# Optimization experiments

Hardware: AMD Instinct MI355X
Metric: run time of the kernel (lower is better)

Reference implementation:

```python
import jax, jax.numpy as jnp
import numpy as np

N_NODES = 50000
N_EDGES = 1600000
IN_C, HID_C, OUT_C = 64, 64, 7


def setup_inputs() -> dict:
    key = jax.random.key(0)
    ks = jax.random.split(key, 8)
    x = jax.random.normal(ks[0], (N_NODES, IN_C), dtype=jnp.float32)
    edge_index = jax.random.randint(ks[1], (2, N_EDGES), 0, N_NODES, dtype=jnp.int64)
    s_in = 1.0 / np.sqrt(IN_C)
    s_hid = 1.0 / np.sqrt(HID_C)
    W1 = jax.random.normal(ks[2], (HID_C, IN_C), dtype=jnp.float32) * s_in
    b1 = jnp.zeros((HID_C,), dtype=jnp.float32)
    W2 = jax.random.normal(ks[3], (HID_C, HID_C), dtype=jnp.float32) * s_hid
    b2 = jnp.zeros((HID_C,), dtype=jnp.float32)
    W3 = jax.random.normal(ks[4], (OUT_C, HID_C), dtype=jnp.float32) * s_hid
    b3 = jnp.zeros((OUT_C,), dtype=jnp.float32)
    return {"x": x, "edge_index": edge_index, "W1": W1, "b1": b1,
            "W2": W2, "b2": b2, "W3": W3, "b3": b3}


def _gcn_conv(x, src, dst, W, b):
    # GCNConv(normalize=False): lin -> sum-aggregate over incoming edges -> +bias
    h = x @ W.T                                   # [N, out]
    msg = h[src]                                  # gather source features [E, out]
    agg = jax.ops.segment_sum(msg, dst, num_segments=N_NODES)  # scatter-add
    return agg + b


def reference(x, edge_index, W1, b1, W2, b2, W3, b3):
    src, dst = edge_index[0], edge_index[1]
    h = jax.nn.relu(_gcn_conv(x, src, dst, W1, b1))   # dropout is identity in eval
    h = jax.nn.relu(_gcn_conv(h, src, dst, W2, b2))
    h = _gcn_conv(h, src, dst, W3, b3)
    return jax.nn.log_softmax(h, axis=-1)
```

## Files before the change

### kernel.cpp

```cpp
#include <hip/hip_runtime.h>
#include <math.h>

#define N_NODES 50000
#define N_EDGES 1600000
#define C 64
#define OUTC 7

#define NB 196
#define BCAP 10240
#define CHUNK 4096

__device__ __forceinline__ unsigned int pk_bf16(float a, float b) {
    unsigned int ua = __float_as_uint(a);
    ua = (ua + 0x7FFFu + ((ua >> 16) & 1u)) >> 16;
    unsigned int ub = __float_as_uint(b);
    ub = (ub + 0x7FFFu + ((ub >> 16) & 1u)) >> 16;
    return ua | (ub << 16);
}

__global__ __launch_bounds__(256) void bin_kernel(const int* __restrict__ src,
                                                  const int* __restrict__ dst,
                                                  unsigned int* __restrict__ buckets,
                                                  int* __restrict__ gcursor) {
    __shared__ unsigned int staged[CHUNK];
    __shared__ int hist[NB], scanb[NB], cur[NB], baseb[NB];
    const int tid = threadIdx.x;
    const int base = blockIdx.x * CHUNK;
    int n = N_EDGES - base; if (n > CHUNK) n = CHUNK;

    for (int b = tid; b < NB; b += 256) { hist[b] = 0; cur[b] = 0; }
    __syncthreads();

    const int4* src4 = (const int4*)(src + base);
    const int4* dst4 = (const int4*)(dst + base);
    unsigned int v[16];
    int nv = n >> 2;
#pragma unroll
    for (int k = 0; k < 4; ++k) {
        int i4 = k * 256 + tid;
        if (i4 < nv) {
            int4 s4 = src4[i4];
            int4 d4 = dst4[i4];
            unsigned int d0 = (unsigned int)d4.x, d1 = (unsigned int)d4.y;
            unsigned int d2 = (unsigned int)d4.z, d3 = (unsigned int)d4.w;
            v[k * 4 + 0] = (d0 << 16) | (unsigned int)s4.x;
            v[k * 4 + 1] = (d1 << 16) | (unsigned int)s4.y;
            v[k * 4 + 2] = (d2 << 16) | (unsigned int)s4.z;
            v[k * 4 + 3] = (d3 << 16) | (unsigned int)s4.w;
            atomicAdd(&hist[d0 >> 8], 1);
            atomicAdd(&hist[d1 >> 8], 1);
            atomicAdd(&hist[d2 >> 8], 1);
            atomicAdd(&hist[d3 >> 8], 1);
        }
    }
    __syncthreads();
    if (tid == 0) {
        int run = 0;
        for (int b = 0; b < NB; ++b) { scanb[b] = run; run += hist[b]; }
    }
    __syncthreads();
#pragma unroll
    for (int k = 0; k < 4; ++k) {
        int i4 = k * 256 + tid;
        if (i4 < nv) {
#pragma unroll
            for (int q = 0; q < 4; ++q) {
                unsigned int w = v[k * 4 + q];
                int b = w >> 24;
                int p = scanb[b] + atomicAdd(&cur[b], 1);
                staged[p] = w;
            }
        }
    }
    __syncthreads();
    if (tid < NB) baseb[tid] = atomicAdd(&gcursor[tid], hist[tid]);
    __syncthreads();
    for (int i = tid; i < n; i += 256) {
        unsigned int w = staged[i];
        int b = w >> 24;
        buckets[(size_t)b * BCAP + baseb[b] + (i - scanb[b])] = w;
    }
}

__global__ __launch_bounds__(256) void build_csr(const unsigned int* __restrict__ buckets,
                                                 const int* __restrict__ gcursor,
                                                 unsigned int* __restrict__ csr,
                                                 int* __restrict__ off) {
    __shared__ int hist[256], part[256], offx[256], cur[256];
    __shared__ int gl[NB];
    __shared__ int s_cnt, s_base;
    const int tid = threadIdx.x;
    const int b = blockIdx.x;

    hist[tid] = 0;
    cur[tid] = 0;
    if (tid < NB) gl[tid] = gcursor[tid];
    __syncthreads();
    if (tid == 0) {
        int bs = 0;
        for (int i = 0; i < b; ++i) bs += gl[i];
        s_base = bs;
        s_cnt = gl[b];
    }
    __syncthreads();
    const int cnt = s_cnt;
    const int gbase = s_base;
    const unsigned int* bk = buckets + (size_t)b * BCAP;

    for (int i = tid; i < cnt; i += 256) {
        atomicAdd(&hist[(bk[i] >> 16) & 255], 1);
    }
    __syncthreads();
    part[tid] = hist[tid];
    __syncthreads();
    for (int d = 1; d < 256; d <<= 1) {
        int t = (tid >= d) ? part[tid - d] : 0;
        __syncthreads();
        part[tid] += t;
        __syncthreads();
    }
    offx[tid] = (tid == 0) ? 0 : part[tid - 1];
    __syncthreads();
    int node = b * 256 + tid;
    if (node < N_NODES) off[node] = gbase + offx[tid];
    if (b == NB - 1 && tid == 0) off[N_NODES] = gbase + cnt;
    for (int i = tid; i < cnt; i += 256) {
        unsigned int w = bk[i];
        int dl = (w >> 16) & 255;
        int p = offx[dl] + atomicAdd(&cur[dl], 1);
        csr[gbase + p] = w & 0xFFFFu;
    }
}


__global__ __launch_bounds__(256) void linear64_bf16(const float* __restrict__ x,
                                                     const float* __restrict__ W,
                                                     unsigned int* __restrict__ tb) {
    const int cg = blockIdx.x & 3;
    const int r = (blockIdx.x >> 2) * 256 + threadIdx.x;
    if (r >= N_NODES) return;
    float4 xr[16];
    const float4* xp = (const float4*)(x + (size_t)r * 64);
#pragma unroll
    for (int j = 0; j < 16; ++j) xr[j] = xp[j];
    const float* xf = (const float*)xr;

    const float* Wp = W + cg * 16 * 64;
    unsigned int* orow = tb + (size_t)r * 32 + cg * 8;
    for (int c0 = 0; c0 < 16; c0 += 8) {
        float acc[8] = {0.f, 0.f, 0.f, 0.f, 0.f, 0.f, 0.f, 0.f};
#pragma unroll
        for (int k = 0; k < 64; ++k) {
            float xv = xf[k];
#pragma unroll
            for (int j = 0; j < 8; ++j)
                acc[j] += xv * Wp[(c0 + j) * 64 + k];
        }
        uint4 w;
        w.x = pk_bf16(acc[0], acc[1]);
        w.y = pk_bf16(acc[2], acc[3]);
        w.z = pk_bf16(acc[4], acc[5]);
        w.w = pk_bf16(acc[6], acc[7]);
        ((uint4*)orow)[c0 >> 3] = w;
    }
}

__global__ __launch_bounds__(128) void linear7_rows(const float* __restrict__ x,
                                                    const float* __restrict__ W,
                                                    float* __restrict__ out) {
    int r = blockIdx.x * 128 + threadIdx.x;
    if (r >= N_NODES) return;
    float4 xr[16];
    const float4* xp = (const float4*)(x + (size_t)r * 64);
#pragma unroll
    for (int j = 0; j < 16; ++j) xr[j] = xp[j];
    const float* xf = (const float*)xr;

    float acc[7] = {0.f, 0.f, 0.f, 0.f, 0.f, 0.f, 0.f};
#pragma unroll
    for (int k = 0; k < 64; ++k) {
        float xv = xf[k];
#pragma unroll
        for (int j = 0; j < 7; ++j)
            acc[j] += xv * W[j * 64 + k];
    }
    float4* op = (float4*)(out + (size_t)r * 8);
    op[0] = make_float4(acc[0], acc[1], acc[2], acc[3]);
    op[1] = make_float4(acc[4], acc[5], acc[6], 0.f);
}


__global__ __launch_bounds__(256) void gather64b(const int* __restrict__ off,
                                                 const unsigned int* __restrict__ csr_src,
                                                 const unsigned int* __restrict__ tb,
                                                 const float* __restrict__ b,
                                                 float* __restrict__ out,
                                                 int do_relu) {
    int node = blockIdx.x * 4 + (threadIdx.x >> 6);
    if (node >= N_NODES) return;
    const int lane = threadIdx.x & 63;
    const int slot = lane >> 3;
    const int ch8  = lane & 7;
    int e0 = off[node], e1 = off[node + 1];
    const uint4* t4 = (const uint4*)tb;
    float s[8] = {0.f, 0.f, 0.f, 0.f, 0.f, 0.f, 0.f, 0.f};
    for (int e = e0; e < e1; e += 16) {
        int i0 = e + slot;
        int i1 = e + 8 + slot;
        bool p0 = i0 < e1, p1 = i1 < e1;
        unsigned int a0 = csr_src[p0 ? i0 : e];
        unsigned int a1 = csr_src[p1 ? i1 : e];
        uint4 v0 = t4[(size_t)a0 * 8 + ch8];
        uint4 v1 = t4[(size_t)a1 * 8 + ch8];
        if (p0) {
            s[0] += __uint_as_float(v0.x << 16);
            s[1] += __uint_as_float(v0.x & 0xFFFF0000u);
            s[2] += __uint_as_float(v0.y << 16);
            s[3] += __uint_as_float(v0.y & 0xFFFF0000u);
            s[4] += __uint_as_float(v0.z << 16);
            s[5] += __uint_as_float(v0.z & 0xFFFF0000u);
            s[6] += __uint_as_float(v0.w << 16);
            s[7] += __uint_as_float(v0.w & 0xFFFF0000u);
        }
        if (p1) {
            s[0] += __uint_as_float(v1.x << 16);
            s[1] += __uint_as_float(v1.x & 0xFFFF0000u);
            s[2] += __uint_as_float(v1.y << 16);
            s[3] += __uint_as_float(v1.y & 0xFFFF0000u);
            s[4] += __uint_as_float(v1.z << 16);
            s[5] += __uint_as_float(v1.z & 0xFFFF0000u);
            s[6] += __uint_as_float(v1.w << 16);
            s[7] += __uint_as_float(v1.w & 0xFFFF0000u);
        }
    }
#pragma unroll
    for (int d = 8; d <= 32; d <<= 1) {
#pragma unroll
        for (int j = 0; j < 8; ++j) s[j] += __shfl_xor(s[j], d, 64);
    }
    if (lane < 8) {
        const float4 b0 = ((const float4*)b)[ch8 * 2];
        const float4 b1 = ((const float4*)b)[ch8 * 2 + 1];
        float4 r0, r1;
        r0.x = s[0] + b0.x; r0.y = s[1] + b0.y; r0.z = s[2] + b0.z; r0.w = s[3] + b0.w;
        r1.x = s[4] + b1.x; r1.y = s[5] + b1.y; r1.z = s[6] + b1.z; r1.w = s[7] + b1.w;
        if (do_relu) {
            r0.x = fmaxf(r0.x, 0.f); r0.y = fmaxf(r0.y, 0.f);
            r0.z = fmaxf(r0.z, 0.f); r0.w = fmaxf(r0.w, 0.f);
            r1.x = fmaxf(r1.x, 0.f); r1.y = fmaxf(r1.y, 0.f);
            r1.z = fmaxf(r1.z, 0.f); r1.w = fmaxf(r1.w, 0.f);
        }
        float4* orow = (float4*)(out + (size_t)node * 64 + ch8 * 8);
        orow[0] = r0;
        orow[1] = r1;
    }
}

__global__ __launch_bounds__(256) void gather7_lsm(const int* __restrict__ off,
                                                   const unsigned int* __restrict__ csr_src,
                                                   const float* __restrict__ t3,
                                                   const float* __restrict__ b,
                                                   float* __restrict__ out) {
    int node = blockIdx.x * 4 + (threadIdx.x >> 6);
    if (node >= N_NODES) return;
    const int lane = threadIdx.x & 63;
    const int slot = lane >> 1;
    const int h    = lane & 1;
    int e0 = off[node], e1 = off[node + 1];
    const float4* t4 = (const float4*)t3;
    float sx = 0.f, sy = 0.f, sz = 0.f, sw = 0.f;
    for (int e = e0 + slot; e < e1; e += 32) {
        unsigned int s = csr_src[e];
        float4 v = t4[(size_t)s * 2 + h];
        sx += v.x; sy += v.y; sz += v.z; sw += v.w;
    }
#pragma unroll
    for (int d = 2; d <= 32; d <<= 1) {
        sx += __shfl_xor(sx, d, 64); sy += __shfl_xor(sy, d, 64);
        sz += __shfl_xor(sz, d, 64); sw += __shfl_xor(sw, d, 64);
    }
    float z0 = sx + b[h * 4 + 0];
    float z1 = sy + b[h * 4 + 1];
    float z2 = sz + b[h * 4 + 2];
    float z3 = (h == 0) ? (sw + b[3]) : -1e30f;
    float m = fmaxf(fmaxf(z0, z1), fmaxf(z2, z3));
    m = fmaxf(m, __shfl_xor(m, 1, 64));
    float ex = __expf(z0 - m) + __expf(z1 - m) + __expf(z2 - m) + __expf(z3 - m);
    ex += __shfl_xor(ex, 1, 64);
    float l = m + __logf(ex);
    if (lane < 2) {
        float* o = out + (size_t)node * 7 + h * 4;
        o[0] = z0 - l; o[1] = z1 - l; o[2] = z2 - l;
        if (h == 0) o[3] = z3 - l;
    }
}

extern "C" void kernel_launch(void* const* d_in, const int* in_sizes, int n_in,
                              void* d_out, int out_size, void* d_ws, size_t ws_size,
                              hipStream_t stream) {
    const float* x  = (const float*)d_in[0];
    const int*   ei = (const int*)d_in[1];
    const float* W1 = (const float*)d_in[2];
    const float* b1 = (const float*)d_in[3];
    const float* W2 = (const float*)d_in[4];
    const float* b2 = (const float*)d_in[5];
    const float* W3 = (const float*)d_in[6];
    const float* b3 = (const float*)d_in[7];
    float* out = (float*)d_out;

    const int* src = ei;
    const int* dst = ei + N_EDGES;

    float* A = (float*)d_ws;
    float* B = A + (size_t)N_NODES * C;
    unsigned int* csr = (unsigned int*)(B + (size_t)N_NODES * C);
    int* off     = (int*)(csr + N_EDGES);
    int* gcursor = off + N_NODES + 8;
    unsigned int* buckets = (unsigned int*)A;
    unsigned int* Abf     = (unsigned int*)A;

    const int l64grid = ((N_NODES + 255) / 256) * 4;
    const int l7grid  = (N_NODES + 127) / 128;
    const int ngrid   = (N_NODES + 3) / 4;

    (void)hipMemsetAsync(gcursor, 0, NB * sizeof(int), stream);
    bin_kernel<<<(N_EDGES + CHUNK - 1) / CHUNK, 256, 0, stream>>>(src, dst, buckets, gcursor);
    build_csr<<<NB, 256, 0, stream>>>(buckets, gcursor, csr, off);

    linear64_bf16<<<l64grid, 256, 0, stream>>>(x, W1, Abf);
    gather64b<<<ngrid, 256, 0, stream>>>(off, csr, Abf, b1, B, 1);

    linear64_bf16<<<l64grid, 256, 0, stream>>>(B, W2, Abf);
    gather64b<<<ngrid, 256, 0, stream>>>(off, csr, Abf, b2, B, 1);

    linear7_rows<<<l7grid, 128, 0, stream>>>(B, W3, A);
    gather7_lsm<<<ngrid, 256, 0, stream>>>(off, csr, A, b3, out);
}
```

Baseline: 264.8 us.

## Split bf16 feature table into two channel halves gathered in separate passes

The linear layer now writes its bf16 output as two planar halves of 32 channels each, and the 64-channel gather is replaced by two launches that each aggregate one half. Each half table is about 3.2 MB instead of 6.4 MB, so a pass's random-access working set is more likely to stay in cache. The cost is reading the CSR index array twice and launching an extra kernel per layer. Each wave now covers 16 edges per iteration with one load per lane instead of two, which lowers memory-level parallelism per thread.

```diff
diff --git a/kernel.cpp b/kernel.cpp
--- a/kernel.cpp
+++ b/kernel.cpp
@@ -9,6 +9,7 @@
 #define NB 196
 #define BCAP 10240
 #define CHUNK 4096
+#define HROW 16
 
 __device__ __forceinline__ unsigned int pk_bf16(float a, float b) {
     unsigned int ua = __float_as_uint(a);
@@ -146,7 +147,8 @@
     const float* xf = (const float*)xr;
 
     const float* Wp = W + cg * 16 * 64;
-    unsigned int* orow = tb + (size_t)r * 32 + cg * 8;
+    unsigned int* orow = tb + (size_t)(cg >> 1) * N_NODES * HROW
+                            + (size_t)r * HROW + (cg & 1) * 8;
     for (int c0 = 0; c0 < 16; c0 += 8) {
         float acc[8] = {0.f, 0.f, 0.f, 0.f, 0.f, 0.f, 0.f, 0.f};
 #pragma unroll
@@ -190,57 +192,45 @@
 }
 
 
-__global__ __launch_bounds__(256) void gather64b(const int* __restrict__ off,
-                                                 const unsigned int* __restrict__ csr_src,
-                                                 const unsigned int* __restrict__ tb,
-                                                 const float* __restrict__ b,
-                                                 float* __restrict__ out,
-                                                 int do_relu) {
+__global__ __launch_bounds__(256) void gather_half(const int* __restrict__ off,
+                                                   const unsigned int* __restrict__ csr_src,
+                                                   const unsigned int* __restrict__ tb,
+                                                   const float* __restrict__ b,
+                                                   float* __restrict__ out,
+                                                   int h, int do_relu) {
     int node = blockIdx.x * 4 + (threadIdx.x >> 6);
     if (node >= N_NODES) return;
     const int lane = threadIdx.x & 63;
-    const int slot = lane >> 3;
-    const int ch8  = lane & 7;
+    const int slot = lane >> 2;
+    const int ch4  = lane & 3;
     int e0 = off[node], e1 = off[node + 1];
-    const uint4* t4 = (const uint4*)tb;
+    const uint4* t4 = (const uint4*)(tb + (size_t)h * N_NODES * HROW);
     float s[8] = {0.f, 0.f, 0.f, 0.f, 0.f, 0.f, 0.f, 0.f};
     for (int e = e0; e < e1; e += 16) {
-        int i0 = e + slot;
-        int i1 = e + 8 + slot;
-        bool p0 = i0 < e1, p1 = i1 < e1;
-        unsigned int a0 = csr_src[p0 ? i0 : e];
-        unsigned int a1 = csr_src[p1 ? i1 : e];
-        uint4 v0 = t4[(size_t)a0 * 8 + ch8];
-        uint4 v1 = t4[(size_t)a1 * 8 + ch8];
-        if (p0) {
-            s[0] += __uint_as_float(v0.x << 16);
-            s[1] += __uint_as_float(v0.x & 0xFFFF0000u);
-            s[2] += __uint_as_float(v0.y << 16);
-            s[3] += __uint_as_float(v0.y & 0xFFFF0000u);
-            s[4] += __uint_as_float(v0.z << 16);
-            s[5] += __uint_as_float(v0.z & 0xFFFF0000u);
-            s[6] += __uint_as_float(v0.w << 16);
-            s[7] += __uint_as_float(v0.w & 0xFFFF0000u);
-        }
-        if (p1) {
-            s[0] += __uint_as_float(v1.x << 16);
-            s[1] += __uint_as_float(v1.x & 0xFFFF0000u);
-            s[2] += __uint_as_float(v1.y << 16);
-            s[3] += __uint_as_float(v1.y & 0xFFFF0000u);
-            s[4] += __uint_as_float(v1.z << 16);
-            s[5] += __uint_as_float(v1.z & 0xFFFF0000u);
-            s[6] += __uint_as_float(v1.w << 16);
-            s[7] += __uint_as_float(v1.w & 0xFFFF0000u);
-        }
-    }
-#pragma unroll
-    for (int d = 8; d <= 32; d <<= 1) {
+        int i = e + slot;
+        bool p = i < e1;
+        unsigned int a = csr_src[p ? i : e];
+        uint4 v = t4[(size_t)a * 4 + ch4];
+        if (p) {
+            s[0] += __uint_as_float(v.x << 16);
+            s[1] += __uint_as_float(v.x & 0xFFFF0000u);
+            s[2] += __uint_as_float(v.y << 16);
+            s[3] += __uint_as_float(v.y & 0xFFFF0000u);
+            s[4] += __uint_as_float(v.z << 16);
+            s[5] += __uint_as_float(v.z & 0xFFFF0000u);
+            s[6] += __uint_as_float(v.w << 16);
+            s[7] += __uint_as_float(v.w & 0xFFFF0000u);
+        }
+    }
+#pragma unroll
+    for (int d = 4; d <= 32; d <<= 1) {
 #pragma unroll
         for (int j = 0; j < 8; ++j) s[j] += __shfl_xor(s[j], d, 64);
     }
-    if (lane < 8) {
-        const float4 b0 = ((const float4*)b)[ch8 * 2];
-        const float4 b1 = ((const float4*)b)[ch8 * 2 + 1];
+    if (lane < 4) {
+        const float* bh = b + h * 32;
+        const float4 b0 = ((const float4*)bh)[ch4 * 2];
+        const float4 b1 = ((const float4*)bh)[ch4 * 2 + 1];
         float4 r0, r1;
         r0.x = s[0] + b0.x; r0.y = s[1] + b0.y; r0.z = s[2] + b0.z; r0.w = s[3] + b0.w;
         r1.x = s[4] + b1.x; r1.y = s[5] + b1.y; r1.z = s[6] + b1.z; r1.w = s[7] + b1.w;
@@ -250,7 +240,7 @@
             r1.x = fmaxf(r1.x, 0.f); r1.y = fmaxf(r1.y, 0.f);
             r1.z = fmaxf(r1.z, 0.f); r1.w = fmaxf(r1.w, 0.f);
         }
-        float4* orow = (float4*)(out + (size_t)node * 64 + ch8 * 8);
+        float4* orow = (float4*)(out + (size_t)node * 64 + h * 32 + ch4 * 8);
         orow[0] = r0;
         orow[1] = r1;
     }
@@ -328,10 +318,12 @@
     build_csr<<<NB, 256, 0, stream>>>(buckets, gcursor, csr, off);
 
     linear64_bf16<<<l64grid, 256, 0, stream>>>(x, W1, Abf);
-    gather64b<<<ngrid, 256, 0, stream>>>(off, csr, Abf, b1, B, 1);
+    gather_half<<<ngrid, 256, 0, stream>>>(off, csr, Abf, b1, B, 0, 1);
+    gather_half<<<ngrid, 256, 0, stream>>>(off, csr, Abf, b1, B, 1, 1);
 
     linear64_bf16<<<l64grid, 256, 0, stream>>>(B, W2, Abf);
-    gather64b<<<ngrid, 256, 0, stream>>>(off, csr, Abf, b2, B, 1);
+    gather_half<<<ngrid, 256, 0, stream>>>(off, csr, Abf, b2, B, 0, 1);
+    gather_half<<<ngrid, 256, 0, stream>>>(off, csr, Abf, b2, B, 1, 1);
 
     linear7_rows<<<l7grid, 128, 0, stream>>>(B, W3, A);
     gather7_lsm<<<ngrid, 256, 0, stream>>>(off, csr, A, b3, out);
```

Result: slower. 299.9 us (+13.3%).
